# Kernel tuning notes

Hardware: AMD Instinct MI355X
Metric: run time of the kernel (lower is better)

## Reference

```python
import jax, jax.numpy as jnp
import numpy as np
import math

H = 16  # n_head
DK = 64  # d_k = n_feat // n_head
BASE = 10000.0


def _rope_cos_sin(T, dk, dtype):
    inv_freq = 1.0 / (BASE ** (jnp.arange(0, dk, 2, dtype=jnp.float32) / dk))
    t = jnp.arange(T, dtype=jnp.float32)
    freqs = jnp.einsum('i,j->ij', t, inv_freq)          # [T, dk/2]
    emb = jnp.concatenate([freqs, freqs], axis=-1)       # [T, dk]
    return jnp.cos(emb).astype(dtype)[:, None, None, :], jnp.sin(emb).astype(dtype)[:, None, None, :]


def _rotate_half(x):
    x1, x2 = jnp.split(x, 2, axis=-1)
    return jnp.concatenate([-x2, x1], axis=-1)


def setup_inputs() -> dict:
    key = jax.random.key(0)
    ks = jax.random.split(key, 8)
    T, B, C = 2048, 2, 1024
    s = 0.02
    return {
        'query': jax.random.normal(ks[0], (T, B, C), jnp.float32),
        'key': jax.random.normal(ks[1], (T, B, C), jnp.float32),
        'value': jax.random.normal(ks[2], (T, B, C), jnp.float32),
        'Wq': jax.random.normal(ks[3], (C, C), jnp.float32) * s,
        'bq': jnp.zeros((C,), jnp.float32),
        'Wk': jax.random.normal(ks[4], (C, C), jnp.float32) * s,
        'bk': jnp.zeros((C,), jnp.float32),
        'Wv': jax.random.normal(ks[5], (C, C), jnp.float32) * s,
        'bv': jnp.zeros((C,), jnp.float32),
        'Wo': jax.random.normal(ks[6], (C, C), jnp.float32) * s,
        'bo': jnp.zeros((C,), jnp.float32),
    }


def reference(query, key, value, Wq, bq, Wk, bk, Wv, bv, Wo, bo):
    T, B, C = value.shape
    # --- RoPE applied to raw inputs (per the original module), before projections ---
    q = query.reshape(T, B, H, DK)
    k = key.reshape(T, B, H, DK)
    cos, sin = _rope_cos_sin(T, DK, q.dtype)  # [T,1,1,DK]
    q = q * cos + _rotate_half(q) * sin
    k = k * cos + _rotate_half(k) * sin
    q = q.reshape(T, B, C).transpose(1, 0, 2)   # [B,T,C]
    k = k.reshape(T, B, C).transpose(1, 0, 2)
    v = value.transpose(1, 0, 2)
    # --- QKV projections (torch Linear: x @ W.T + b) ---
    q = (jnp.einsum('btc,dc->btd', q, Wq) + bq).reshape(B, T, H, DK).transpose(0, 2, 1, 3)
    k = (jnp.einsum('btc,dc->btd', k, Wk) + bk).reshape(B, T, H, DK).transpose(0, 2, 1, 3)
    v = (jnp.einsum('btc,dc->btd', v, Wv) + bv).reshape(B, T, H, DK).transpose(0, 2, 1, 3)
    # --- scaled dot-product attention ---
    scores = jnp.einsum('bhqd,bhkd->bhqk', q, k) / math.sqrt(DK)
    attn = jax.nn.softmax(scores, axis=-1)
    x = jnp.einsum('bhqk,bhkd->bhqd', attn, v)        # [B,H,T,DK]
    x = x.transpose(0, 2, 1, 3).reshape(B, T, C)
    out = jnp.einsum('btc,dc->btd', x, Wo) + bo        # [B,T,C]
    return out.transpose(1, 0, 2)                      # [T,B,C]
```

## Files before the change

kernel.cpp:

```cpp
#include <hip/hip_runtime.h>
#include <hip/hip_bf16.h>
#include <math.h>

#define T_SEQ 2048
#define B_SZ 2
#define C_DIM 1024
#define H_HEADS 16
#define DKH 64
#define M_ROWS (T_SEQ * B_SZ)

#define QSCALE 0.1803368801111204f

typedef __attribute__((ext_vector_type(8))) short bf16x8;
typedef __attribute__((ext_vector_type(4))) float f32x4;
typedef unsigned short ushort_t;


__device__ __forceinline__ ushort_t f2bf(float f) {
    unsigned u = __float_as_uint(f);
    u += 0x7fffu + ((u >> 16) & 1u);
    return (ushort_t)(u >> 16);
}

__device__ __forceinline__ unsigned pack2bf(float a, float b) {
#if __has_builtin(__builtin_amdgcn_cvt_pk_bf16_f32)
    typedef __attribute__((ext_vector_type(2))) __bf16 bf16x2_t;
    union { bf16x2_t v; unsigned u; } cv;
    cv.v = __builtin_amdgcn_cvt_pk_bf16_f32(a, b);
    return cv.u;
#else
    return (unsigned)f2bf(a) | ((unsigned)f2bf(b) << 16);
#endif
}

__device__ __forceinline__ void async_copy16(const void* g, void* l) {
    __builtin_amdgcn_global_load_lds(
        (const __attribute__((address_space(1))) void*)g,
        (__attribute__((address_space(3))) void*)l, 16, 0, 0);
}

__global__ __launch_bounds__(256) void prep_all(
        const float* __restrict__ q, const float* __restrict__ k,
        const float* __restrict__ value,
        const float* __restrict__ Wq, const float* __restrict__ Wk,
        const float* __restrict__ Wv, const float* __restrict__ Wo,
        ushort_t* __restrict__ qb, ushort_t* __restrict__ kb,
        ushort_t* __restrict__ vb2,
        ushort_t* __restrict__ Wqb, ushort_t* __restrict__ Wkb,
        ushort_t* __restrict__ Wvb, ushort_t* __restrict__ Wob) {
    int bid = blockIdx.x;
    int tid = threadIdx.x;
    if (bid < 8192) {
        int idx  = bid * 256 + tid;
        int j    = idx & 31;
        int rest = idx >> 5;
        int h    = rest & (H_HEADS - 1);
        int tb   = rest >> 4;
        int t    = tb >> 1;
        float inv = exp2f(-(float)j * 0.41524101186092034f);
        float ang = (float)t * inv;
        float s, c;
        sincosf(ang, &s, &c);
        int base = tb * C_DIM + h * DKH + j;
        float q1 = q[base], q2 = q[base + 32];
        float k1 = k[base], k2 = k[base + 32];
        qb[base]      = f2bf(q1 * c - q2 * s);
        qb[base + 32] = f2bf(q2 * c + q1 * s);
        kb[base]      = f2bf(k1 * c - k2 * s);
        kb[base + 32] = f2bf(k2 * c + k1 * s);
    } else if (bid < 12288) {
        int i   = (bid - 8192) * 256 + tid;
        int c4  = i & 255;
        int row = i >> 8;
        int b   = row >> 11, t = row & 2047;
        float4 v = reinterpret_cast<const float4*>(value)[(t * 2 + b) * 256 + c4];
        ushort4 o;
        o.x = f2bf(v.x); o.y = f2bf(v.y); o.z = f2bf(v.z); o.w = f2bf(v.w);
        reinterpret_cast<ushort4*>(vb2)[i] = o;
    } else {
        int r     = bid - 12288;
        int which = r >> 10;
        int i     = (r & 1023) * 256 + tid;
        const float* in = which == 0 ? Wq : which == 1 ? Wk : which == 2 ? Wv : Wo;
        ushort_t*   out = which == 0 ? Wqb : which == 1 ? Wkb : which == 2 ? Wvb : Wob;
        float4 v = reinterpret_cast<const float4*>(in)[i];
        ushort4 o;
        o.x = f2bf(v.x); o.y = f2bf(v.y); o.z = f2bf(v.z); o.w = f2bf(v.w);
        reinterpret_cast<ushort4*>(out)[i] = o;
    }
}

__device__ __forceinline__ void gemm_core(
        ushort_t* AsBase, ushort_t* BsBase,
        const ushort_t* __restrict__ A, const ushort_t* __restrict__ W,
        const float* __restrict__ bias, void* __restrict__ Cout,
        int N, int K, float scale, int rowBase, int colBase,
        bool biasRow, bool bf16out) {
    const int tid  = threadIdx.x;
    const int lane = tid & 63;
    const int w    = tid >> 6;
    const int m16  = lane & 15, quad = lane >> 4;
    const int r8   = lane >> 3, c8 = lane & 7;
    const int clog = c8 ^ r8;

    f32x4 acc[4];
#pragma unroll
    for (int j = 0; j < 4; j++) acc[j] = (f32x4){0.f, 0.f, 0.f, 0.f};

    auto stage = [&](int buf, int kt) {
#pragma unroll
        for (int i = 0; i < 2; ++i) {
            int R = w * 16 + i * 8;
            async_copy16(A + (size_t)(rowBase + R + r8) * K + kt + clog * 8,
                         AsBase + buf * 8192 + R * 64);
        }
        {
            int R = w * 8;
            async_copy16(W + (size_t)(colBase + R + r8) * K + kt + clog * 8,
                         BsBase + buf * 4096 + R * 64);
        }
    };

    stage(0, 0);
    int cur = 0;
    for (int kt = 0; kt < K; kt += 64, cur ^= 1) {
        if (kt + 64 < K) {
            stage(cur ^ 1, kt + 64);
            asm volatile("s_waitcnt vmcnt(3)" ::: "memory");
        } else {
            asm volatile("s_waitcnt vmcnt(0)" ::: "memory");
        }
        __builtin_amdgcn_s_barrier();
        __builtin_amdgcn_sched_barrier(0);
        const ushort_t* Asc = AsBase + cur * 8192;
        const ushort_t* Bsc = BsBase + cur * 4096;
#pragma unroll
        for (int ks = 0; ks < 2; ++ks) {
            int lc = ks * 4 + quad;
            bf16x8 af;
            {
                int R = w * 16 + m16;
                af = *reinterpret_cast<const bf16x8*>(
                    &Asc[R * 64 + ((lc ^ (R & 7)) << 3)]);
            }
            bf16x8 bfr[4];
#pragma unroll
            for (int ni = 0; ni < 4; ni++) {
                int R = ni * 16 + m16;
                bfr[ni] = *reinterpret_cast<const bf16x8*>(
                    &Bsc[R * 64 + ((lc ^ (R & 7)) << 3)]);
            }
#pragma unroll
            for (int ni = 0; ni < 4; ni++)
                acc[ni] = __builtin_amdgcn_mfma_f32_16x16x32_bf16(
                    af, bfr[ni], acc[ni], 0, 0, 0);
        }
        __builtin_amdgcn_s_barrier();
    }
#pragma unroll
    for (int ni = 0; ni < 4; ni++)
#pragma unroll
        for (int r = 0; r < 4; r++) {
            int row = rowBase + w * 16 + quad * 4 + r;
            int col = colBase + ni * 16 + m16;
            float v = (acc[ni][r] + (biasRow ? bias[row] : bias[col])) * scale;
            if (bf16out)
                ((ushort_t*)Cout)[(size_t)row * N + col] = f2bf(v);
            else
                ((float*)Cout)[(size_t)row * N + col] = v;
        }
}

__global__ __launch_bounds__(512) void qkv_gemm(
        const ushort_t* __restrict__ qb, const ushort_t* __restrict__ kb,
        const ushort_t* __restrict__ Wqb, const ushort_t* __restrict__ Wkb,
        const ushort_t* __restrict__ Wvb, const ushort_t* __restrict__ vb2,
        const float* __restrict__ bq, const float* __restrict__ bk,
        const float* __restrict__ bv,
        ushort_t* __restrict__ Qp, ushort_t* __restrict__ Kp,
        ushort_t* __restrict__ VTg) {
    __shared__ ushort_t As[2][128 * 64];
    __shared__ ushort_t Bs[2][64 * 64];
    int z = blockIdx.y;
    const ushort_t* A; const ushort_t* W; const float* bias; ushort_t* C;
    int N, bx, by; bool biasRow; float scale;
    if (z == 0) {
        A = qb;  W = Wqb; bias = bq; C = Qp;  N = C_DIM;  biasRow = false;
        scale = QSCALE; bx = blockIdx.x & 15; by = blockIdx.x >> 4;
    } else if (z == 1) {
        A = kb;  W = Wkb; bias = bk; C = Kp;  N = C_DIM;  biasRow = false;
        scale = 1.0f;   bx = blockIdx.x & 15; by = blockIdx.x >> 4;
    } else {
        A = Wvb; W = vb2; bias = bv; C = VTg; N = M_ROWS; biasRow = true;
        scale = 1.0f;   bx = blockIdx.x & 63; by = blockIdx.x >> 6;
    }
    gemm_core(&As[0][0], &Bs[0][0], A, W, bias, C, N, C_DIM, scale,
              by * 128, bx * 64, biasRow, true);
}

__global__ __launch_bounds__(512) void gemm_o(
        const ushort_t* __restrict__ Xb, const ushort_t* __restrict__ Wob,
        const float* __restrict__ bo, float* __restrict__ out) {
    __shared__ ushort_t As[2][128 * 64];
    __shared__ ushort_t Bs[2][64 * 64];
    gemm_core(&As[0][0], &Bs[0][0], Xb, Wob, bo, out, C_DIM, C_DIM, 1.0f,
              blockIdx.y * 128, blockIdx.x * 64, false, false);
}

__global__ __launch_bounds__(256) void attn(
        const ushort_t* __restrict__ Qp, const ushort_t* __restrict__ Kp,
        const ushort_t* __restrict__ VTg, ushort_t* __restrict__ X) {
    __shared__ char smem[32768];
    char*  KtC   = smem;
    char*  VTC   = smem + 16384;
    ushort_t* Qt = (ushort_t*)(smem + 16384);
    float* exch  = (float*)smem;
    float* lbuf  = (float*)smem;

    const int tid  = threadIdx.x;
    const int lane = tid & 63;
    const int w    = tid >> 6;
    const int m16  = lane & 15, quad = lane >> 4;
    const int r8   = lane >> 3, c8 = lane & 7;
    const int clog = c8 ^ r8;

    const int lid   = blockIdx.x + blockIdx.y * 32;
    const int jj    = lid >> 3;
    const int pair  = (lid & 7) * 4 + (jj >> 5);
    const int qBase = (jj & 31) * 64;
    const int b = pair >> 4, h = pair & 15;

    const int ofA = m16 * 128 + ((quad ^ (m16 & 7)) << 4);
    const int ofB = m16 * 128 + (((4 + quad) ^ (m16 & 7)) << 4);
    const int sw4 = (m16 >> 1) & 3;
    const int fro = m16 * 64 + ((quad ^ sw4) << 4);
    int pw0[2];
#pragma unroll
    for (int kt_i = 0; kt_i < 2; kt_i++)
        pw0[kt_i] = m16 * 64 + (((kt_i * 2 + (quad >> 1)) ^ sw4) << 4) + (quad & 1) * 8;
    char* PwC = KtC + w * 4096;

    const int vlc = (lane & 3) ^ ((lane >> 3) & 3);

    auto stageK = [&](int kt) {
#pragma unroll
        for (int i = 0; i < 4; ++i) {
            int key = kt + w * 32 + i * 8 + r8;
            async_copy16(Kp + (size_t)(key * 2 + b) * C_DIM + h * DKH + clog * 8,
                         KtC + w * 4096 + i * 1024);
        }
    };
    auto stageV = [&](int kt) {
#pragma unroll
        for (int i = 0; i < 4; ++i) {
            int dkr = i * 16 + (lane >> 2);
            async_copy16(VTg + (size_t)(h * DKH + dkr) * M_ROWS + b * T_SEQ + kt + w * 32 + vlc * 8,
                         VTC + w * 4096 + i * 1024);
        }
    };

#pragma unroll
    for (int i = 0; i < 2; ++i) {
        int R = w * 16 + i * 8;
        async_copy16(Qp + (size_t)((qBase + R + r8) * 2 + b) * C_DIM + h * DKH + clog * 8,
                     &Qt[R * 64]);
    }
    stageK(0);
    asm volatile("s_waitcnt vmcnt(4)" ::: "memory");
    __builtin_amdgcn_s_barrier();
    bf16x8 aq[4][2];
#pragma unroll
    for (int ni = 0; ni < 4; ni++) {
        aq[ni][0] = *reinterpret_cast<const bf16x8*>((const char*)Qt + ni * 2048 + ofA);
        aq[ni][1] = *reinterpret_cast<const bf16x8*>((const char*)Qt + ni * 2048 + ofB);
    }
    asm volatile("s_waitcnt lgkmcnt(0)" ::: "memory");
    __builtin_amdgcn_s_barrier();
    stageV(0);

    float lrun[4] = {0.f, 0.f, 0.f, 0.f};
    f32x4 o[4][4];
#pragma unroll
    for (int mi = 0; mi < 4; mi++)
#pragma unroll
        for (int ni = 0; ni < 4; ni++) o[mi][ni] = (f32x4){0.f, 0.f, 0.f, 0.f};

    for (int kt = 0; kt < T_SEQ; kt += 128) {
        asm volatile("s_waitcnt vmcnt(0)" ::: "memory");
        __builtin_amdgcn_sched_barrier(0);

        f32x4 s[2][4];
#pragma unroll
        for (int kt_i = 0; kt_i < 2; kt_i++) {
#pragma unroll
            for (int ni = 0; ni < 4; ni++) s[kt_i][ni] = (f32x4){0.f, 0.f, 0.f, 0.f};
            bf16x8 kf0 = *reinterpret_cast<const bf16x8*>(KtC + w * 4096 + kt_i * 2048 + ofA);
            bf16x8 kf1 = *reinterpret_cast<const bf16x8*>(KtC + w * 4096 + kt_i * 2048 + ofB);
#pragma unroll
            for (int ni = 0; ni < 4; ni++) {
                s[kt_i][ni] = __builtin_amdgcn_mfma_f32_16x16x32_bf16(kf0, aq[ni][0], s[kt_i][ni], 0, 0, 0);
                s[kt_i][ni] = __builtin_amdgcn_mfma_f32_16x16x32_bf16(kf1, aq[ni][1], s[kt_i][ni], 0, 0, 0);
            }
        }

#pragma unroll
        for (int kt_i = 0; kt_i < 2; kt_i++)
#pragma unroll
            for (int ni = 0; ni < 4; ni++) {
                float p0 = __builtin_amdgcn_exp2f(s[kt_i][ni][0]);
                float p1 = __builtin_amdgcn_exp2f(s[kt_i][ni][1]);
                float p2 = __builtin_amdgcn_exp2f(s[kt_i][ni][2]);
                float p3 = __builtin_amdgcn_exp2f(s[kt_i][ni][3]);
                lrun[ni] += (p0 + p1) + (p2 + p3);
                uint2 pv;
                pv.x = pack2bf(p0, p1);
                pv.y = pack2bf(p2, p3);
                *reinterpret_cast<uint2*>(PwC + ni * 1024 + pw0[kt_i]) = pv;
            }
        asm volatile("s_waitcnt lgkmcnt(0)" ::: "memory");

        bf16x8 pf[4];
#pragma unroll
        for (int ni = 0; ni < 4; ni++)
            pf[ni] = *reinterpret_cast<const bf16x8*>(PwC + ni * 1024 + fro);
        bf16x8 vfr[4];
#pragma unroll
        for (int mi = 0; mi < 4; mi++)
            vfr[mi] = *reinterpret_cast<const bf16x8*>(VTC + w * 4096 + mi * 1024 + fro);
        asm volatile("s_waitcnt lgkmcnt(0)" ::: "memory");
        __builtin_amdgcn_sched_barrier(0);
        if (kt + 128 < T_SEQ) { stageK(kt + 128); stageV(kt + 128); }
        __builtin_amdgcn_sched_barrier(0);

#pragma unroll
        for (int mi = 0; mi < 4; mi++)
#pragma unroll
            for (int ni = 0; ni < 4; ni++)
                o[mi][ni] = __builtin_amdgcn_mfma_f32_16x16x32_bf16(vfr[mi], pf[ni], o[mi][ni], 0, 0, 0);
    }

#pragma unroll
    for (int ni = 0; ni < 4; ni++) {
        lrun[ni] += __shfl_xor(lrun[ni], 16);
        lrun[ni] += __shfl_xor(lrun[ni], 32);
    }
    float lv = quad == 0 ? lrun[0] : quad == 1 ? lrun[1] : quad == 2 ? lrun[2] : lrun[3];

    __syncthreads();
    lbuf[w * 64 + quad * 16 + m16] = lv;
    __syncthreads();
    const int qq = tid >> 2;
    const float invl = 1.0f / (lbuf[qq] + lbuf[64 + qq] + lbuf[128 + qq] + lbuf[192 + qq]);
    __syncthreads();

#pragma unroll
    for (int rnd = 0; rnd < 2; rnd++) {
        if (rnd) __syncthreads();
#pragma unroll
        for (int t2 = 0; t2 < 2; t2++) {
            int mi = 2 * rnd + t2;
#pragma unroll
            for (int ni = 0; ni < 4; ni++) {
                int q = ni * 16 + m16;
                int cw = t2 * 4 + quad;
                *reinterpret_cast<f32x4*>(
                    &exch[w * 2048 + q * 32 + ((cw ^ (q & 7)) << 2)]) = o[mi][ni];
            }
        }
        __syncthreads();
#pragma unroll
        for (int half = 0; half < 2; half++) {
            int c = (tid & 3) + 4 * half;
            int off = qq * 32 + (((c ^ (qq & 7))) << 2);
            f32x4 v = *reinterpret_cast<const f32x4*>(&exch[off]);
            f32x4 v1 = *reinterpret_cast<const f32x4*>(&exch[2048 + off]);
            f32x4 v2 = *reinterpret_cast<const f32x4*>(&exch[4096 + off]);
            f32x4 v3 = *reinterpret_cast<const f32x4*>(&exch[6144 + off]);
            v = v + v1 + v2 + v3;
            uint2 pk;
            pk.x = pack2bf(v[0] * invl, v[1] * invl);
            pk.y = pack2bf(v[2] * invl, v[3] * invl);
            int t = qBase + qq;
            *reinterpret_cast<uint2*>(
                &X[(size_t)(t * 2 + b) * C_DIM + h * DKH + rnd * 32 + c * 4]) = pk;
        }
    }
}

extern "C" void kernel_launch(void* const* d_in, const int* in_sizes, int n_in,
                              void* d_out, int out_size, void* d_ws, size_t ws_size,
                              hipStream_t stream) {
    const float* query = (const float*)d_in[0];
    const float* key   = (const float*)d_in[1];
    const float* value = (const float*)d_in[2];
    const float* Wq = (const float*)d_in[3];
    const float* bq = (const float*)d_in[4];
    const float* Wk = (const float*)d_in[5];
    const float* bk = (const float*)d_in[6];
    const float* Wv = (const float*)d_in[7];
    const float* bv = (const float*)d_in[8];
    const float* Wo = (const float*)d_in[9];
    const float* bo = (const float*)d_in[10];
    float* out = (float*)d_out;

    ushort_t* qb  = (ushort_t*)d_ws;
    ushort_t* kb  = qb  + (size_t)M_ROWS * C_DIM;
    ushort_t* vb2 = kb  + (size_t)M_ROWS * C_DIM;
    ushort_t* Wqb = vb2 + (size_t)M_ROWS * C_DIM;
    ushort_t* Wkb = Wqb + (size_t)C_DIM * C_DIM;
    ushort_t* Wvb = Wkb + (size_t)C_DIM * C_DIM;
    ushort_t* Wob = Wvb + (size_t)C_DIM * C_DIM;
    ushort_t* Qp  = Wob + (size_t)C_DIM * C_DIM;
    ushort_t* Kp  = Qp  + (size_t)M_ROWS * C_DIM;
    ushort_t* VTg = Kp  + (size_t)M_ROWS * C_DIM;
    ushort_t* Xb  = VTg + (size_t)M_ROWS * C_DIM;

    prep_all<<<16384, 256, 0, stream>>>(query, key, value, Wq, Wk, Wv, Wo,
                                        qb, kb, vb2, Wqb, Wkb, Wvb, Wob);

    qkv_gemm<<<dim3(512, 3), 512, 0, stream>>>(qb, kb, Wqb, Wkb, Wvb, vb2,
                                               bq, bk, bv, Qp, Kp, VTg);

    attn<<<dim3(T_SEQ / 64, B_SZ * H_HEADS), 256, 0, stream>>>(Qp, Kp, VTg, Xb);

    gemm_o<<<dim3(C_DIM / 64, M_ROWS / 128), 512, 0, stream>>>(Xb, Wob, bo, out);
}
```

Measured before the change: 225.3 us.

## Enlarge GEMM block tile to 128x128 with 2x4 MFMA per-wave subtiles

Widens the shared GEMM core tile from 128x64 to 128x128, arranging the 8 waves as a 4x2 grid where each wave computes a 32x64 subtile with 8 accumulators. The B-tile LDS buffers double, staging issues two loads per thread for B, and the wait count and grid sizes are adjusted to match. The aim is more MFMA work per LDS fragment load and less redundant global traffic. In exchange it uses more LDS and registers and launches half as many blocks (768 for QKV, 256 for the output GEMM), which may underfill the GPU.

```diff
diff --git a/kernel.cpp b/kernel.cpp
--- a/kernel.cpp
+++ b/kernel.cpp
@@ -99,13 +99,17 @@
     const int tid  = threadIdx.x;
     const int lane = tid & 63;
     const int w    = tid >> 6;
+    const int rowg = w >> 1;
+    const int colg = w & 1;
     const int m16  = lane & 15, quad = lane >> 4;
     const int r8   = lane >> 3, c8 = lane & 7;
     const int clog = c8 ^ r8;
 
-    f32x4 acc[4];
-#pragma unroll
-    for (int j = 0; j < 4; j++) acc[j] = (f32x4){0.f, 0.f, 0.f, 0.f};
+    f32x4 acc[2][4];
+#pragma unroll
+    for (int mi = 0; mi < 2; mi++)
+#pragma unroll
+        for (int ni = 0; ni < 4; ni++) acc[mi][ni] = (f32x4){0.f, 0.f, 0.f, 0.f};
 
     auto stage = [&](int buf, int kt) {
 #pragma unroll
@@ -114,10 +118,11 @@
             async_copy16(A + (size_t)(rowBase + R + r8) * K + kt + clog * 8,
                          AsBase + buf * 8192 + R * 64);
         }
-        {
-            int R = w * 8;
+#pragma unroll
+        for (int i = 0; i < 2; ++i) {
+            int R = w * 16 + i * 8;
             async_copy16(W + (size_t)(colBase + R + r8) * K + kt + clog * 8,
-                         BsBase + buf * 4096 + R * 64);
+                         BsBase + buf * 8192 + R * 64);
         }
     };
 
@@ -126,49 +131,54 @@
     for (int kt = 0; kt < K; kt += 64, cur ^= 1) {
         if (kt + 64 < K) {
             stage(cur ^ 1, kt + 64);
-            asm volatile("s_waitcnt vmcnt(3)" ::: "memory");
+            asm volatile("s_waitcnt vmcnt(4)" ::: "memory");
         } else {
             asm volatile("s_waitcnt vmcnt(0)" ::: "memory");
         }
         __builtin_amdgcn_s_barrier();
         __builtin_amdgcn_sched_barrier(0);
         const ushort_t* Asc = AsBase + cur * 8192;
-        const ushort_t* Bsc = BsBase + cur * 4096;
+        const ushort_t* Bsc = BsBase + cur * 8192;
 #pragma unroll
         for (int ks = 0; ks < 2; ++ks) {
             int lc = ks * 4 + quad;
-            bf16x8 af;
-            {
-                int R = w * 16 + m16;
-                af = *reinterpret_cast<const bf16x8*>(
+            bf16x8 af[2];
+#pragma unroll
+            for (int mi = 0; mi < 2; mi++) {
+                int R = rowg * 32 + mi * 16 + m16;
+                af[mi] = *reinterpret_cast<const bf16x8*>(
                     &Asc[R * 64 + ((lc ^ (R & 7)) << 3)]);
             }
             bf16x8 bfr[4];
 #pragma unroll
             for (int ni = 0; ni < 4; ni++) {
-                int R = ni * 16 + m16;
+                int R = colg * 64 + ni * 16 + m16;
                 bfr[ni] = *reinterpret_cast<const bf16x8*>(
                     &Bsc[R * 64 + ((lc ^ (R & 7)) << 3)]);
             }
 #pragma unroll
-            for (int ni = 0; ni < 4; ni++)
-                acc[ni] = __builtin_amdgcn_mfma_f32_16x16x32_bf16(
-                    af, bfr[ni], acc[ni], 0, 0, 0);
+            for (int mi = 0; mi < 2; mi++)
+#pragma unroll
+                for (int ni = 0; ni < 4; ni++)
+                    acc[mi][ni] = __builtin_amdgcn_mfma_f32_16x16x32_bf16(
+                        af[mi], bfr[ni], acc[mi][ni], 0, 0, 0);
         }
         __builtin_amdgcn_s_barrier();
     }
 #pragma unroll
-    for (int ni = 0; ni < 4; ni++)
-#pragma unroll
-        for (int r = 0; r < 4; r++) {
-            int row = rowBase + w * 16 + quad * 4 + r;
-            int col = colBase + ni * 16 + m16;
-            float v = (acc[ni][r] + (biasRow ? bias[row] : bias[col])) * scale;
-            if (bf16out)
-                ((ushort_t*)Cout)[(size_t)row * N + col] = f2bf(v);
-            else
-                ((float*)Cout)[(size_t)row * N + col] = v;
-        }
+    for (int mi = 0; mi < 2; mi++)
+#pragma unroll
+        for (int ni = 0; ni < 4; ni++)
+#pragma unroll
+            for (int r = 0; r < 4; r++) {
+                int row = rowBase + rowg * 32 + mi * 16 + quad * 4 + r;
+                int col = colBase + colg * 64 + ni * 16 + m16;
+                float v = (acc[mi][ni][r] + (biasRow ? bias[row] : bias[col])) * scale;
+                if (bf16out)
+                    ((ushort_t*)Cout)[(size_t)row * N + col] = f2bf(v);
+                else
+                    ((float*)Cout)[(size_t)row * N + col] = v;
+            }
 }
 
 __global__ __launch_bounds__(512) void qkv_gemm(
@@ -180,31 +190,31 @@
         ushort_t* __restrict__ Qp, ushort_t* __restrict__ Kp,
         ushort_t* __restrict__ VTg) {
     __shared__ ushort_t As[2][128 * 64];
-    __shared__ ushort_t Bs[2][64 * 64];
+    __shared__ ushort_t Bs[2][128 * 64];
     int z = blockIdx.y;
     const ushort_t* A; const ushort_t* W; const float* bias; ushort_t* C;
     int N, bx, by; bool biasRow; float scale;
     if (z == 0) {
         A = qb;  W = Wqb; bias = bq; C = Qp;  N = C_DIM;  biasRow = false;
-        scale = QSCALE; bx = blockIdx.x & 15; by = blockIdx.x >> 4;
+        scale = QSCALE; bx = blockIdx.x & 7;  by = blockIdx.x >> 3;
     } else if (z == 1) {
         A = kb;  W = Wkb; bias = bk; C = Kp;  N = C_DIM;  biasRow = false;
-        scale = 1.0f;   bx = blockIdx.x & 15; by = blockIdx.x >> 4;
+        scale = 1.0f;   bx = blockIdx.x & 7;  by = blockIdx.x >> 3;
     } else {
         A = Wvb; W = vb2; bias = bv; C = VTg; N = M_ROWS; biasRow = true;
-        scale = 1.0f;   bx = blockIdx.x & 63; by = blockIdx.x >> 6;
+        scale = 1.0f;   bx = blockIdx.x & 31; by = blockIdx.x >> 5;
     }
     gemm_core(&As[0][0], &Bs[0][0], A, W, bias, C, N, C_DIM, scale,
-              by * 128, bx * 64, biasRow, true);
+              by * 128, bx * 128, biasRow, true);
 }
 
 __global__ __launch_bounds__(512) void gemm_o(
         const ushort_t* __restrict__ Xb, const ushort_t* __restrict__ Wob,
         const float* __restrict__ bo, float* __restrict__ out) {
     __shared__ ushort_t As[2][128 * 64];
-    __shared__ ushort_t Bs[2][64 * 64];
+    __shared__ ushort_t Bs[2][128 * 64];
     gemm_core(&As[0][0], &Bs[0][0], Xb, Wob, bo, out, C_DIM, C_DIM, 1.0f,
-              blockIdx.y * 128, blockIdx.x * 64, false, false);
+              blockIdx.y * 128, blockIdx.x * 128, false, false);
 }
 
 __global__ __launch_bounds__(256) void attn(
@@ -418,10 +428,10 @@
     prep_all<<<16384, 256, 0, stream>>>(query, key, value, Wq, Wk, Wv, Wo,
                                         qb, kb, vb2, Wqb, Wkb, Wvb, Wob);
 
-    qkv_gemm<<<dim3(512, 3), 512, 0, stream>>>(qb, kb, Wqb, Wkb, Wvb, vb2,
+    qkv_gemm<<<dim3(256, 3), 512, 0, stream>>>(qb, kb, Wqb, Wkb, Wvb, vb2,
                                                bq, bk, bv, Qp, Kp, VTg);
 
     attn<<<dim3(T_SEQ / 64, B_SZ * H_HEADS), 256, 0, stream>>>(Qp, Kp, VTg, Xb);
 
-    gemm_o<<<dim3(C_DIM / 64, M_ROWS / 128), 512, 0, stream>>>(Xb, Wob, bo, out);
-}
+    gemm_o<<<dim3(C_DIM / 128, M_ROWS / 128), 512, 0, stream>>>(Xb, Wob, bo, out);
+}
```

New measurement: 229.4 us. No clear change (+1.8%).
